# Performance work log

Measured on AMD Instinct MI355X. Metric: run time of the kernel, lower is better.

The kernel has to match this reference:

```python
import jax, jax.numpy as jnp
import numpy as np

B, S, D = 1, 4096, 512      # batch, seq, model dim
E, K, H = 64, 2, 256        # routed experts, top-k, expert hidden (moe_inter_dim)
HS = 2048                   # shared expert hidden = n_shared_experts * inter_dim
EPS = 1e-5                  # LayerNorm eps (torch default)


def setup_inputs() -> dict:
    key = jax.random.key(0)
    ks = jax.random.split(key, 16)
    n = lambda k, shp, s=0.02: jax.random.normal(k, shp, dtype=jnp.float32) * s
    return {
        "x": jax.random.normal(ks[0], (B, S, D), dtype=jnp.float32),
        # gate Linear(dim -> E)
        "Wg": n(ks[1], (E, D)), "bg": n(ks[2], (E,)),
        # per-expert LayerNorm affine
        "gamma": 1.0 + n(ks[3], (E, D)), "beta": n(ks[4], (E, D)),
        # per-expert SwiGLU: w1, w3: D->H ; w2: H->D
        "W1": n(ks[5], (E, D, H)), "b1": n(ks[6], (E, H)),
        "W3": n(ks[7], (E, D, H)), "b3": n(ks[8], (E, H)),
        "W2": n(ks[9], (E, H, D)), "b2": n(ks[10], (E, D)),
        # shared expert (same Expert structure, hidden HS)
        "gs": 1.0 + n(ks[11], (D,)), "bs": n(ks[11], (D,)),
        "Ws1": n(ks[12], (D, HS)), "bs1": n(ks[12], (HS,)),
        "Ws3": n(ks[13], (D, HS)), "bs3": n(ks[13], (HS,)),
        "Ws2": n(ks[14], (HS, D)), "bs2": n(ks[15], (D,)),
    }


def reference(x, Wg, bg, gamma, beta, W1, b1, W3, b3, W2, b2,
              gs, bs, Ws1, bs1, Ws3, bs3, Ws2, bs2):
    shape = x.shape
    xt = x.reshape(-1, D)                      # [T, D] tokens
    T = xt.shape[0]

    # ---- Gate (eval path: sigmoid scores, no load balancing / bias / groups) ----
    scores = jax.nn.sigmoid(xt @ Wg.T + bg)    # [T, E]
    w, idx = jax.lax.top_k(scores, K)          # [T, K]
    w = w / w.sum(-1, keepdims=True)           # sigmoid path normalization; route_scale = 1
    # dense combine weights: cw[t, e] = routing weight of token t on expert e (0 if not routed)
    cw = jnp.zeros((T, E), xt.dtype).at[jnp.arange(T)[:, None], idx].add(w)

    # ---- Shared LayerNorm statistics (affine folded per-expert below) ----
    mu = xt.mean(-1, keepdims=True)
    var = ((xt - mu) ** 2).mean(-1, keepdims=True)
    nx = (xt - mu) * jax.lax.rsqrt(var + EPS)  # [T, D], unit-affine normalized

    # Fold each expert's LN affine (gamma_e, beta_e) into its w1/w3:
    # (nx*g + b) @ W = nx @ (g[:,None]*W) + b @ W
    W1p = gamma[:, :, None] * W1
    b1p = b1 + jnp.einsum('ed,edh->eh', beta, W1)
    W3p = gamma[:, :, None] * W3
    b3p = b3 + jnp.einsum('ed,edh->eh', beta, W3)

    h1 = jnp.einsum('td,edh->eth', nx, W1p) + b1p[:, None, :]   # [E, T, H]
    h3 = jnp.einsum('td,edh->eth', nx, W3p) + b3p[:, None, :]
    h = jax.nn.silu(h1) * h3                                     # SwiGLU, [E, T, H]

    # Weighted combine: y[t] = sum_e cw[t,e] * (h[e,t] @ W2[e] + b2[e])
    hw = h * cw.T[:, :, None]                                    # [E, T, H]
    y = jnp.einsum('eth,ehd->td', hw, W2) + cw @ b2              # [T, D]

    # ---- Shared expert (applied to every token) ----
    nxs = nx * gs + bs
    hs = jax.nn.silu(nxs @ Ws1 + bs1) * (nxs @ Ws3 + bs3)        # [T, HS]
    z = hs @ Ws2 + bs2

    return (y + z).reshape(shape)
```

## Files before the change

### kernel.cpp

```cpp
#include <hip/hip_runtime.h>
#include <math.h>

typedef unsigned short u16;
typedef __attribute__((ext_vector_type(8))) short bf16x8;
typedef __attribute__((ext_vector_type(4))) float f32x4;

#define TT   4096
#define DM   512
#define NE   64
#define HE   256
#define HSH  2048
#define NSH  8
#define PADBASE 16384
#define MAXTILES 384
#define MAXRT    128

__device__ __forceinline__ float sig_(float z){ return 1.f/(1.f+__expf(-z)); }

__device__ __forceinline__ u16 f2bf(float x){
  unsigned int u = __builtin_bit_cast(unsigned int, x);
  u = (u + 0x7FFFu + ((u >> 16) & 1u)) >> 16;
  return (u16)u;
}

__device__ __forceinline__ f32x4 mfma16(bf16x8 a, bf16x8 b, f32x4 c){
  return __builtin_amdgcn_mfma_f32_16x16x32_bf16(a, b, c, 0, 0, 0);
}

__device__ __forceinline__ bf16x8 frd(const char* tile, int row, int q){
  return *(const bf16x8*)(tile + row*64 + q*16);
}

__device__ __forceinline__ void gl16(const void* g, void* l){
  __builtin_amdgcn_global_load_lds(
      (const __attribute__((address_space(1))) unsigned int*)g,
      (__attribute__((address_space(3))) unsigned int*)l, 16, 0, 0);
}

__global__ __launch_bounds__(256) void k_cvtT(
    const float* __restrict__ in, const float* __restrict__ scale,
    const float* __restrict__ foldvec, u16* __restrict__ out,
    float* __restrict__ foldout, int K, int N)
{
  __shared__ u16 T[64][80];
  __shared__ float red[64][65];
  const int tid = threadIdx.x;
  const int k0 = blockIdx.x*64, n0 = blockIdx.y*64;
  const float* ip = in + (size_t)blockIdx.z * K * N;
  const int r = tid>>2, cb = (tid&3)*16;
  const float sc = scale   ? scale[(size_t)blockIdx.z*K + k0 + r]   : 1.0f;
  const float fv = foldvec ? foldvec[(size_t)blockIdx.z*K + k0 + r] : 0.0f;
  #pragma unroll
  for (int j = 0; j < 4; j++){
    float4 v = *(const float4*)(ip + (size_t)(k0+r)*N + n0 + cb + j*4);
    T[cb+j*4+0][r] = f2bf(v.x*sc);
    T[cb+j*4+1][r] = f2bf(v.y*sc);
    T[cb+j*4+2][r] = f2bf(v.z*sc);
    T[cb+j*4+3][r] = f2bf(v.w*sc);
    if (foldout){
      red[cb+j*4+0][r] = v.x*fv;
      red[cb+j*4+1][r] = v.y*fv;
      red[cb+j*4+2][r] = v.z*fv;
      red[cb+j*4+3][r] = v.w*fv;
    }
  }
  __syncthreads();
  if (foldout){
    const int c = tid & 63, rq = tid >> 6;
    float s = 0.f;
    #pragma unroll
    for (int rr = 0; rr < 16; rr++) s += red[c][rq*16 + rr];
    atomicAdd(foldout + (size_t)blockIdx.z*N + n0 + c, s);
  }
  const int n = tid>>2, kb = (tid&3)*16;
  uint4 a = *(const uint4*)&T[n][kb];
  uint4 b = *(const uint4*)&T[n][kb+8];
  u16* op = out + (size_t)blockIdx.z*K*N;
  *(uint4*)(op + (size_t)(n0+n)*K + k0 + kb)     = a;
  *(uint4*)(op + (size_t)(n0+n)*K + k0 + kb + 8) = b;
}

__global__ __launch_bounds__(256) void k_ln_gate(
    const float* __restrict__ x, const float* __restrict__ Wg, const float* __restrict__ bg,
    u16* __restrict__ nxb, int* __restrict__ top_idx, float* __restrict__ top_w)
{
  __shared__ float xs[DM];
  __shared__ float sred[4], ssred[4];
  __shared__ float sc[NE];
  const int tid = threadIdx.x;
  const int t   = blockIdx.x;

  float2 v = reinterpret_cast<const float2*>(x + (size_t)t*DM)[tid];
  xs[2*tid]   = v.x;
  xs[2*tid+1] = v.y;
  float s  = v.x + v.y;
  float ss = v.x*v.x + v.y*v.y;
  #pragma unroll
  for (int o = 32; o > 0; o >>= 1){ s += __shfl_xor(s, o); ss += __shfl_xor(ss, o); }
  const int wid = tid >> 6, lane = tid & 63;
  if (lane == 0){ sred[wid] = s; ssred[wid] = ss; }
  __syncthreads();
  const float tot = sred[0]+sred[1]+sred[2]+sred[3];
  const float tss = ssred[0]+ssred[1]+ssred[2]+ssred[3];
  const float mu  = tot * (1.f/DM);
  const float var = tss * (1.f/DM) - mu*mu;
  const float rstd = rsqrtf(var + 1e-5f);
  unsigned int pk = (unsigned int)f2bf((v.x-mu)*rstd) | ((unsigned int)f2bf((v.y-mu)*rstd) << 16);
  *(unsigned int*)(nxb + (size_t)t*DM + 2*tid) = pk;

  const int e = tid >> 2, sub = tid & 3;
  const float4* wrow4 = reinterpret_cast<const float4*>(Wg + (size_t)e*DM);
  const float4* xs4   = reinterpret_cast<const float4*>(xs);
  float acc = 0.f;
  #pragma unroll 4
  for (int i = sub; i < DM/4; i += 4){
    const float4 w = wrow4[i]; const float4 xv = xs4[i];
    acc += xv.x*w.x + xv.y*w.y + xv.z*w.z + xv.w*w.w;
  }
  acc += __shfl_xor(acc, 1);
  acc += __shfl_xor(acc, 2);
  if (sub == 0) sc[e] = acc + bg[e];
  __syncthreads();

  if (tid < 64) {
    const float s0 = sc[tid];
    float m = s0; int mi = tid;
    #pragma unroll
    for (int o = 1; o < 64; o <<= 1){
      float om = __shfl_xor(m, o); int oi = __shfl_xor(mi, o);
      if (om > m || (om == m && oi < mi)) { m = om; mi = oi; }
    }
    float s1 = (tid == mi) ? -INFINITY : s0;
    float m2 = s1; int mi2 = tid;
    #pragma unroll
    for (int o = 1; o < 64; o <<= 1){
      float om = __shfl_xor(m2, o); int oi = __shfl_xor(mi2, o);
      if (om > m2 || (om == m2 && oi < mi2)) { m2 = om; mi2 = oi; }
    }
    if (tid == 0){
      const float w0 = sig_(m), w1 = sig_(m2);
      const float inv = 1.f/(w0+w1);
      top_idx[2*t]   = mi;
      top_idx[2*t+1] = mi2;
      top_w[2*t]     = w0*inv;
      top_w[2*t+1]   = w1*inv;
    }
  }
}

__global__ __launch_bounds__(256) void k_route(
    const int* __restrict__ top_idx, const float* __restrict__ top_w,
    int* __restrict__ bucket_tok, float* __restrict__ bucket_w,
    int* __restrict__ tiles, int* __restrict__ n_tiles)
{
  __shared__ int cnt[NE], base_[NE];
  __shared__ int nroute;
  const int tid = threadIdx.x;
  if (tid < NE) cnt[tid] = 0;
  __syncthreads();
  for (int p = tid; p < TT*2; p += 256) atomicAdd(&cnt[top_idx[p]], 1);
  __syncthreads();
  if (tid == 0){
    int run = 0, ntl = 0;
    for (int e = 0; e < NE; e++){
      base_[e] = run;
      const int c = cnt[e];
      for (int b = 0; b < c; b += 128){
        const int n = (c - b < 128) ? (c - b) : 128;
        tiles[ntl++] = (e << 17) | (((run + b) >> 7) << 8) | n;
      }
      run += ((c + 127) >> 7) << 7;
    }
    nroute = ntl;
    n_tiles[0] = ntl + NSH*(TT/128);
    n_tiles[1] = ntl;
  }
  __syncthreads();
  if (tid < NSH*(TT/128)){
    const int s = tid >> 5, t = tid & 31;
    const int b0 = PADBASE + s*TT + t*128;
    tiles[nroute + tid] = ((NE + s) << 17) | ((b0 >> 7) << 8) | 128;
  }
  if (tid < NE) cnt[tid] = 0;
  __syncthreads();
  for (int p = tid; p < TT*2; p += 256){
    const int e = top_idx[p];
    const int pos = base_[e] + atomicAdd(&cnt[e], 1);
    bucket_tok[pos] = p >> 1;
    bucket_w[pos]   = top_w[p];
  }
}

__global__ __launch_bounds__(512) void k_up(
    const u16* __restrict__ nxb,
    const u16* __restrict__ W1bT, const u16* __restrict__ W3bT,
    const u16* __restrict__ Ws1bT, const u16* __restrict__ Ws3bT,
    const float* __restrict__ b1, const float* __restrict__ b3,
    const float* __restrict__ bs1, const float* __restrict__ bs3,
    const float* __restrict__ b1f, const float* __restrict__ b3f,
    const int* __restrict__ bucket_tok, const float* __restrict__ bucket_w,
    const int* __restrict__ tiles, const int* __restrict__ n_tiles,
    u16* __restrict__ hrout, u16* __restrict__ hs)
{
  if ((int)blockIdx.x >= n_tiles[0]) return;
  const int info = tiles[blockIdx.x];
  const int e  = info >> 17;
  const int b0 = ((info >> 8) & 0x1FF) << 7;
  const int nt = info & 255;
  const bool sh = (e >= NE);
  const int y  = blockIdx.y;

  __shared__ __align__(16) char Ab[2][8192];
  __shared__ __align__(16) char B1b[2][8192];
  __shared__ __align__(16) char B3b[2][8192];
  __shared__ int   toks[128];
  __shared__ float tw[128];

  const int tid = threadIdx.x, wid = tid >> 6, lane = tid & 63;
  const int l15 = lane & 15, q = lane >> 4;

  if (tid < 128){
    int tk; float w;
    if (!sh){
      if (tid < nt){ tk = bucket_tok[b0+tid]; w = bucket_w[b0+tid]; }
      else         { tk = 0; w = 0.f; }
    } else {
      tk = ((b0 - PADBASE) & (TT-1)) + tid; w = 1.f;
    }
    toks[tid] = tk; tw[tid] = w;
  }
  __syncthreads();

  const u16* w1e = sh ? (Ws1bT + (size_t)(e-NE)*HE*DM) : (W1bT + (size_t)e*HE*DM);
  const u16* w3e = sh ? (Ws3bT + (size_t)(e-NE)*HE*DM) : (W3bT + (size_t)e*HE*DM);

  const int srow = lane >> 2, soff = (lane & 3)*8;
  const u16* asrc = nxb + (size_t)toks[wid*16 + srow]*DM + soff;
  const u16* b1s  = w1e + (size_t)(y*128 + wid*16 + srow)*DM + soff;
  const u16* b3s  = w3e + (size_t)(y*128 + wid*16 + srow)*DM + soff;
  const int loff = wid*1024;

#define UP_STAGE(ph, k0) do{ \
    gl16(asrc + (k0), Ab[ph] + loff); \
    gl16(b1s  + (k0), B1b[ph] + loff); \
    gl16(b3s  + (k0), B3b[ph] + loff); \
  } while(0)

  const int wm = (wid & 1)*64, wn = (wid >> 1)*32;

  const float* ob1 = sh ? (bs1 + (size_t)(e-NE)*HE) : (b1 + (size_t)e*HE);
  const float* ob3 = sh ? (bs3 + (size_t)(e-NE)*HE) : (b3 + (size_t)e*HE);
  f32x4 acc1[4][2], acc3[4][2];
  #pragma unroll
  for (int fn = 0; fn < 2; fn++){
    const int h = y*128 + wn + fn*16 + l15;
    const float v1 = ob1[h] + b1f[(size_t)e*HE + h];
    const float v3 = ob3[h] + b3f[(size_t)e*HE + h];
    #pragma unroll
    for (int fm = 0; fm < 4; fm++){
      acc1[fm][fn] = (f32x4){v1,v1,v1,v1};
      acc3[fm][fn] = (f32x4){v3,v3,v3,v3};
    }
  }

  UP_STAGE(0, 0);
  __syncthreads();

  for (int ks = 0; ks < DM/32; ks++){
    const int cur = ks & 1;
    if (ks < DM/32 - 1) UP_STAGE(cur^1, (ks+1)*32);
    const char* A  = Ab[cur];
    const char* B1 = B1b[cur];
    const char* B3 = B3b[cur];
    bf16x8 fa[4];
    #pragma unroll
    for (int fm = 0; fm < 4; fm++) fa[fm] = frd(A, wm + fm*16 + l15, q);
    #pragma unroll
    for (int fn = 0; fn < 2; fn++){
      bf16x8 fb1 = frd(B1, wn + fn*16 + l15, q);
      bf16x8 fb3 = frd(B3, wn + fn*16 + l15, q);
      #pragma unroll
      for (int fm = 0; fm < 4; fm++){
        acc1[fm][fn] = mfma16(fa[fm], fb1, acc1[fm][fn]);
        acc3[fm][fn] = mfma16(fa[fm], fb3, acc3[fm][fn]);
      }
    }
    __syncthreads();
  }
#undef UP_STAGE

  const int tbase = sh ? ((b0 - PADBASE) & (TT-1)) : 0;
  const int scol  = sh ? (e - NE)*HE : 0;
  #pragma unroll
  for (int fm = 0; fm < 4; fm++){
    #pragma unroll
    for (int fn = 0; fn < 2; fn++){
      const int hl = y*128 + wn + fn*16 + l15;
      #pragma unroll
      for (int r = 0; r < 4; r++){
        const int m = wm + fm*16 + 4*q + r;
        float v = 0.f;
        if (m < nt){
          const float a1 = acc1[fm][fn][r];
          const float a3 = acc3[fm][fn][r];
          v = a1 * sig_(a1) * a3 * tw[m];
        }
        if (sh) hs[(size_t)(tbase+m)*HSH + scol + hl] = f2bf(v);
        else    hrout[(size_t)(b0+m)*HE + hl] = f2bf(v);
      }
    }
  }
}

__global__ __launch_bounds__(256) void k_down_shared(
    const u16* __restrict__ hs, const u16* __restrict__ Ws2bT,
    const float* __restrict__ bs2, float* __restrict__ out)
{
  __shared__ __align__(16) char Ab[2][4096];
  __shared__ __align__(16) char Bb[2][8192];

  const int tid = threadIdx.x, wid = tid >> 6, lane = tid & 63;
  const int l15 = lane & 15, q = lane >> 4;
  const int t0 = blockIdx.x*64, d0 = blockIdx.y*128;

  const int srow = tid >> 2, soff = (tid & 3)*8;
  const u16* asrc  = hs    + (size_t)(t0 + srow)*HSH + soff;
  const u16* bsrc0 = Ws2bT + (size_t)(d0 + srow)*HSH + soff;
  const u16* bsrc1 = Ws2bT + (size_t)(d0 + 64 + srow)*HSH + soff;
  const int loff = wid*1024;

#define DS_STAGE(ph, k0) do{ \
    gl16(asrc  + (k0), Ab[ph] + loff); \
    gl16(bsrc0 + (k0), Bb[ph] + loff); \
    gl16(bsrc1 + (k0), Bb[ph] + 4096 + loff); \
  } while(0)

  const int wm = (wid & 1)*32, wn = (wid >> 1)*64;

  f32x4 acc[2][4];
  #pragma unroll
  for (int fm = 0; fm < 2; fm++)
    #pragma unroll
    for (int fn = 0; fn < 4; fn++) acc[fm][fn] = (f32x4){0.f,0.f,0.f,0.f};

  DS_STAGE(0, 0);
  __syncthreads();

  for (int ks = 0; ks < HSH/32; ks++){
    const int cur = ks & 1;
    if (ks < HSH/32 - 1) DS_STAGE(cur^1, (ks+1)*32);
    const char* A = Ab[cur];
    const char* B = Bb[cur];
    bf16x8 fa[2];
    #pragma unroll
    for (int fm = 0; fm < 2; fm++) fa[fm] = frd(A, wm + fm*16 + l15, q);
    #pragma unroll
    for (int fn = 0; fn < 4; fn++){
      bf16x8 fb = frd(B, wn + fn*16 + l15, q);
      #pragma unroll
      for (int fm = 0; fm < 2; fm++)
        acc[fm][fn] = mfma16(fa[fm], fb, acc[fm][fn]);
    }
    __syncthreads();
  }
#undef DS_STAGE

  #pragma unroll
  for (int fm = 0; fm < 2; fm++){
    #pragma unroll
    for (int fn = 0; fn < 4; fn++){
      const int d = d0 + wn + fn*16 + l15;
      const float bv = bs2[d];
      #pragma unroll
      for (int r = 0; r < 4; r++){
        const int t = t0 + wm + fm*16 + 4*q + r;
        out[(size_t)t*DM + d] = acc[fm][fn][r] + bv;
      }
    }
  }
}

__global__ __launch_bounds__(512) void k_down_routed(
    const u16* __restrict__ hrout, const u16* __restrict__ W2bT,
    const float* __restrict__ b2,
    const int* __restrict__ bucket_tok, const float* __restrict__ bucket_w,
    const int* __restrict__ tiles, const int* __restrict__ n_tiles,
    float* __restrict__ out)
{
  if ((int)blockIdx.x >= n_tiles[1]) return;
  const int info = tiles[blockIdx.x];
  const int e  = info >> 17;
  const int b0 = ((info >> 8) & 0x1FF) << 7;
  const int nt = info & 255;
  const int d0 = blockIdx.y * 256;

  __shared__ __align__(16) char Ab[2][8192];
  __shared__ __align__(16) char Bb[2][16384];
  __shared__ int   toks[128];
  __shared__ float tw[128];

  const int tid = threadIdx.x, wid = tid >> 6, lane = tid & 63;
  const int l15 = lane & 15, q = lane >> 4;

  if (tid < 128){
    if (tid < nt){ toks[tid] = bucket_tok[b0+tid]; tw[tid] = bucket_w[b0+tid]; }
    else         { toks[tid] = 0; tw[tid] = 0.f; }
  }
  __syncthreads();

  const u16* w2e = W2bT + (size_t)e*DM*HE;
  const int srow = tid >> 2, soff = (tid & 3)*8;
  const u16* asrc  = hrout + (size_t)(b0 + srow)*HE + soff;
  const u16* bsrc0 = w2e + (size_t)(d0 + srow)*HE + soff;
  const u16* bsrc1 = w2e + (size_t)(d0 + 128 + srow)*HE + soff;
  const int loff = wid*1024;

#define DR_STAGE(ph, k0) do{ \
    gl16(asrc  + (k0), Ab[ph] + loff); \
    gl16(bsrc0 + (k0), Bb[ph] + loff); \
    gl16(bsrc1 + (k0), Bb[ph] + 8192 + loff); \
  } while(0)

  const int wm = (wid & 1)*64, wn = (wid >> 1)*64;

  f32x4 acc[4][4];
  #pragma unroll
  for (int fm = 0; fm < 4; fm++)
    #pragma unroll
    for (int fn = 0; fn < 4; fn++) acc[fm][fn] = (f32x4){0.f,0.f,0.f,0.f};

  DR_STAGE(0, 0);
  __syncthreads();

  for (int ks = 0; ks < HE/32; ks++){
    const int cur = ks & 1;
    if (ks < HE/32 - 1) DR_STAGE(cur^1, (ks+1)*32);
    const char* A = Ab[cur];
    const char* B = Bb[cur];
    bf16x8 fa[4];
    #pragma unroll
    for (int fm = 0; fm < 4; fm++) fa[fm] = frd(A, wm + fm*16 + l15, q);
    #pragma unroll
    for (int fn = 0; fn < 4; fn++){
      bf16x8 fb = frd(B, wn + fn*16 + l15, q);
      #pragma unroll
      for (int fm = 0; fm < 4; fm++)
        acc[fm][fn] = mfma16(fa[fm], fb, acc[fm][fn]);
    }
    __syncthreads();
  }
#undef DR_STAGE

  #pragma unroll
  for (int fm = 0; fm < 4; fm++){
    #pragma unroll
    for (int fn = 0; fn < 4; fn++){
      const int d = d0 + wn + fn*16 + l15;
      #pragma unroll
      for (int r = 0; r < 4; r++){
        const int m = wm + fm*16 + 4*q + r;
        if (m < nt)
          atomicAdd(out + (size_t)toks[m]*DM + d, acc[fm][fn][r] + tw[m]*b2[(size_t)e*DM + d]);
      }
    }
  }
}

extern "C" void kernel_launch(void* const* d_in, const int* in_sizes, int n_in,
                              void* d_out, int out_size, void* d_ws, size_t ws_size,
                              hipStream_t stream)
{
  (void)in_sizes; (void)n_in; (void)ws_size; (void)out_size;
  const float* x     = (const float*)d_in[0];
  const float* Wg    = (const float*)d_in[1];
  const float* bg    = (const float*)d_in[2];
  const float* gamma = (const float*)d_in[3];
  const float* beta  = (const float*)d_in[4];
  const float* W1    = (const float*)d_in[5];
  const float* b1    = (const float*)d_in[6];
  const float* W3    = (const float*)d_in[7];
  const float* b3    = (const float*)d_in[8];
  const float* W2    = (const float*)d_in[9];
  const float* b2    = (const float*)d_in[10];
  const float* gs    = (const float*)d_in[11];
  const float* bs    = (const float*)d_in[12];
  const float* Ws1   = (const float*)d_in[13];
  const float* bs1   = (const float*)d_in[14];
  const float* Ws3   = (const float*)d_in[15];
  const float* bs3   = (const float*)d_in[16];
  const float* Ws2   = (const float*)d_in[17];
  const float* bs2   = (const float*)d_in[18];
  float* out = (float*)d_out;

  char* ws = (char*)d_ws;
  size_t off = 0;
  auto alloc = [&](size_t bytes) -> char* {
    char* p = ws + off;
    off += (bytes + 255) & ~(size_t)255;
    return p;
  };
  u16*   nxb        = (u16*)  alloc((size_t)TT*DM*2);
  int*   top_idx    = (int*)  alloc((size_t)TT*2*4);
  float* top_w      = (float*)alloc((size_t)TT*2*4);
  int*   bucket_tok = (int*)  alloc((size_t)PADBASE*4);
  float* bucket_w   = (float*)alloc((size_t)PADBASE*4);
  int*   tiles      = (int*)  alloc(MAXTILES*4);
  int*   n_tiles    = (int*)  alloc(64);
  u16*   hrout      = (u16*)  alloc((size_t)PADBASE*HE*2);
  u16*   hs         = (u16*)  alloc((size_t)TT*HSH*2);
  u16*   W1bT       = (u16*)  alloc((size_t)NE*HE*DM*2);
  u16*   W3bT       = (u16*)  alloc((size_t)NE*HE*DM*2);
  u16*   W2bT       = (u16*)  alloc((size_t)NE*DM*HE*2);
  u16*   Ws1bT      = (u16*)  alloc((size_t)HSH*DM*2);
  u16*   Ws3bT      = (u16*)  alloc((size_t)HSH*DM*2);
  u16*   Ws2bT      = (u16*)  alloc((size_t)DM*HSH*2);
  float* b1f        = (float*)alloc((size_t)(NE*HE + HSH)*4);
  float* b3f        = (float*)alloc((size_t)(NE*HE + HSH)*4);

  hipMemsetAsync(b1f, 0, (size_t)(NE*HE + HSH)*4, stream);
  hipMemsetAsync(b3f, 0, (size_t)(NE*HE + HSH)*4, stream);
  k_cvtT<<<dim3(DM/64, HE/64, NE), 256, 0, stream>>>(W1, gamma, beta, W1bT, b1f, DM, HE);
  k_cvtT<<<dim3(DM/64, HE/64, NE), 256, 0, stream>>>(W3, gamma, beta, W3bT, b3f, DM, HE);
  k_cvtT<<<dim3(HE/64, DM/64, NE), 256, 0, stream>>>(W2, nullptr, nullptr, W2bT, nullptr, HE, DM);
  k_cvtT<<<dim3(DM/64, HSH/64, 1), 256, 0, stream>>>(Ws1, gs, bs, Ws1bT, b1f + NE*HE, DM, HSH);
  k_cvtT<<<dim3(DM/64, HSH/64, 1), 256, 0, stream>>>(Ws3, gs, bs, Ws3bT, b3f + NE*HE, DM, HSH);
  k_cvtT<<<dim3(HSH/64, DM/64, 1), 256, 0, stream>>>(Ws2, nullptr, nullptr, Ws2bT, nullptr, HSH, DM);

  k_ln_gate<<<dim3(TT), 256, 0, stream>>>(x, Wg, bg, nxb, top_idx, top_w);
  k_route<<<dim3(1), 256, 0, stream>>>(top_idx, top_w, bucket_tok, bucket_w, tiles, n_tiles);

  k_up<<<dim3(MAXTILES, 2), 512, 0, stream>>>(nxb, W1bT, W3bT, Ws1bT, Ws3bT,
                                              b1, b3, bs1, bs3, b1f, b3f,
                                              bucket_tok, bucket_w, tiles, n_tiles, hrout, hs);
  k_down_shared<<<dim3(TT/64, DM/128), 256, 0, stream>>>(hs, Ws2bT, bs2, out);
  k_down_routed<<<dim3(MAXRT, 2), 512, 0, stream>>>(hrout, W2bT, b2,
                                                    bucket_tok, bucket_w, tiles, n_tiles, out);
}
```

Before: 226.1 us.

## Triple-buffer GEMM loads, swizzle LDS tiles, fuse weight conversion launches

Each of the three GEMM kernels now keeps three LDS stages in flight. It waits with explicit vmcnt counts and raw barriers instead of __syncthreads, and raises wave priority around the MFMA block, so global loads overlap compute more deeply. The LDS column index is XOR-swizzled on both the global-to-LDS copy and the fragment reads to reduce bank conflicts. The six weight conversion/transposition launches are merged into one grid that dispatches by block index, cutting launch overhead. These changes raise LDS use per block, which may lower occupancy, and they depend on hand-counted waitcnt values being correct.

Result: faster. 204.9 us (-9.4%).

```diff
diff --git a/kernel.cpp b/kernel.cpp
--- a/kernel.cpp
+++ b/kernel.cpp
@@ -15,6 +15,10 @@
 #define MAXTILES 384
 #define MAXRT    128
 
+#define WAITV(N) asm volatile("s_waitcnt vmcnt(" #N ")" ::: "memory")
+#define SBAR()   __builtin_amdgcn_s_barrier()
+#define SCHEDB() __builtin_amdgcn_sched_barrier(0)
+
 __device__ __forceinline__ float sig_(float z){ return 1.f/(1.f+__expf(-z)); }
 
 __device__ __forceinline__ u16 f2bf(float x){
@@ -27,8 +31,8 @@
   return __builtin_amdgcn_mfma_f32_16x16x32_bf16(a, b, c, 0, 0, 0);
 }
 
-__device__ __forceinline__ bf16x8 frd(const char* tile, int row, int q){
-  return *(const bf16x8*)(tile + row*64 + q*16);
+__device__ __forceinline__ bf16x8 frd(const char* tile, int row, int csw){
+  return *(const bf16x8*)(tile + row*64 + csw);
 }
 
 __device__ __forceinline__ void gl16(const void* g, void* l){
@@ -37,47 +41,61 @@
       (__attribute__((address_space(3))) unsigned int*)l, 16, 0, 0);
 }
 
-__global__ __launch_bounds__(256) void k_cvtT(
-    const float* __restrict__ in, const float* __restrict__ scale,
-    const float* __restrict__ foldvec, u16* __restrict__ out,
-    float* __restrict__ foldout, int K, int N)
-{
+struct CvtJob {
+  const float* in; const float* scale; const float* fvec;
+  u16* out; float* fout; int K; int N; int base;
+};
+struct CvtJobs { CvtJob j[6]; };
+
+__global__ __launch_bounds__(256) void k_cvt_all(CvtJobs jobs)
+{
+  const int bid = blockIdx.x;
+  int ji = 0;
+  #pragma unroll
+  for (int i = 1; i < 6; i++) ji = (bid >= jobs.j[i].base) ? i : ji;
+  const CvtJob J = jobs.j[ji];
+  const int local = bid - J.base;
+  const int nbx = J.K >> 6, nby = J.N >> 6;
+  const int pm = nbx * nby;
+  const int z = local / pm, rem = local - z*pm;
+  const int bx = rem % nbx, by = rem / nbx;
+
   __shared__ u16 T[64][80];
   __shared__ float red[64][65];
   const int tid = threadIdx.x;
-  const int k0 = blockIdx.x*64, n0 = blockIdx.y*64;
-  const float* ip = in + (size_t)blockIdx.z * K * N;
+  const int k0 = bx*64, n0 = by*64;
+  const float* ip = J.in + (size_t)z * J.K * J.N;
   const int r = tid>>2, cb = (tid&3)*16;
-  const float sc = scale   ? scale[(size_t)blockIdx.z*K + k0 + r]   : 1.0f;
-  const float fv = foldvec ? foldvec[(size_t)blockIdx.z*K + k0 + r] : 0.0f;
-  #pragma unroll
-  for (int j = 0; j < 4; j++){
-    float4 v = *(const float4*)(ip + (size_t)(k0+r)*N + n0 + cb + j*4);
-    T[cb+j*4+0][r] = f2bf(v.x*sc);
-    T[cb+j*4+1][r] = f2bf(v.y*sc);
-    T[cb+j*4+2][r] = f2bf(v.z*sc);
-    T[cb+j*4+3][r] = f2bf(v.w*sc);
-    if (foldout){
-      red[cb+j*4+0][r] = v.x*fv;
-      red[cb+j*4+1][r] = v.y*fv;
-      red[cb+j*4+2][r] = v.z*fv;
-      red[cb+j*4+3][r] = v.w*fv;
-    }
-  }
-  __syncthreads();
-  if (foldout){
+  const float sc = J.scale ? J.scale[(size_t)z*J.K + k0 + r] : 1.0f;
+  const float fv = J.fvec  ? J.fvec [(size_t)z*J.K + k0 + r] : 0.0f;
+  #pragma unroll
+  for (int jj = 0; jj < 4; jj++){
+    float4 v = *(const float4*)(ip + (size_t)(k0+r)*J.N + n0 + cb + jj*4);
+    T[cb+jj*4+0][r] = f2bf(v.x*sc);
+    T[cb+jj*4+1][r] = f2bf(v.y*sc);
+    T[cb+jj*4+2][r] = f2bf(v.z*sc);
+    T[cb+jj*4+3][r] = f2bf(v.w*sc);
+    if (J.fout){
+      red[cb+jj*4+0][r] = v.x*fv;
+      red[cb+jj*4+1][r] = v.y*fv;
+      red[cb+jj*4+2][r] = v.z*fv;
+      red[cb+jj*4+3][r] = v.w*fv;
+    }
+  }
+  __syncthreads();
+  if (J.fout){
     const int c = tid & 63, rq = tid >> 6;
     float s = 0.f;
     #pragma unroll
     for (int rr = 0; rr < 16; rr++) s += red[c][rq*16 + rr];
-    atomicAdd(foldout + (size_t)blockIdx.z*N + n0 + c, s);
+    atomicAdd(J.fout + (size_t)z*J.N + n0 + c, s);
   }
   const int n = tid>>2, kb = (tid&3)*16;
   uint4 a = *(const uint4*)&T[n][kb];
   uint4 b = *(const uint4*)&T[n][kb+8];
-  u16* op = out + (size_t)blockIdx.z*K*N;
-  *(uint4*)(op + (size_t)(n0+n)*K + k0 + kb)     = a;
-  *(uint4*)(op + (size_t)(n0+n)*K + k0 + kb + 8) = b;
+  u16* op = J.out + (size_t)z*J.K*J.N;
+  *(uint4*)(op + (size_t)(n0+n)*J.K + k0 + kb)     = a;
+  *(uint4*)(op + (size_t)(n0+n)*J.K + k0 + kb + 8) = b;
 }
 
 __global__ __launch_bounds__(256) void k_ln_gate(
@@ -210,9 +228,9 @@
   const bool sh = (e >= NE);
   const int y  = blockIdx.y;
 
-  __shared__ __align__(16) char Ab[2][8192];
-  __shared__ __align__(16) char B1b[2][8192];
-  __shared__ __align__(16) char B3b[2][8192];
+  __shared__ __align__(16) char Ab[3][8192];
+  __shared__ __align__(16) char B1b[3][8192];
+  __shared__ __align__(16) char B3b[3][8192];
   __shared__ int   toks[128];
   __shared__ float tw[128];
 
@@ -234,10 +252,11 @@
   const u16* w1e = sh ? (Ws1bT + (size_t)(e-NE)*HE*DM) : (W1bT + (size_t)e*HE*DM);
   const u16* w3e = sh ? (Ws3bT + (size_t)(e-NE)*HE*DM) : (W3bT + (size_t)e*HE*DM);
 
-  const int srow = lane >> 2, soff = (lane & 3)*8;
-  const u16* asrc = nxb + (size_t)toks[wid*16 + srow]*DM + soff;
-  const u16* b1s  = w1e + (size_t)(y*128 + wid*16 + srow)*DM + soff;
-  const u16* b3s  = w3e + (size_t)(y*128 + wid*16 + srow)*DM + soff;
+  const int srow = lane >> 2;
+  const int csrc = (((lane & 3) ^ ((lane >> 3) & 3))) * 8;
+  const u16* asrc = nxb + (size_t)toks[wid*16 + srow]*DM + csrc;
+  const u16* b1s  = w1e + (size_t)(y*128 + wid*16 + srow)*DM + csrc;
+  const u16* b3s  = w3e + (size_t)(y*128 + wid*16 + srow)*DM + csrc;
   const int loff = wid*1024;
 
 #define UP_STAGE(ph, k0) do{ \
@@ -264,28 +283,36 @@
   }
 
   UP_STAGE(0, 0);
-  __syncthreads();
+  UP_STAGE(1, 32);
+  const int csw = (q ^ ((l15 >> 1) & 3)) * 16;
 
   for (int ks = 0; ks < DM/32; ks++){
-    const int cur = ks & 1;
-    if (ks < DM/32 - 1) UP_STAGE(cur^1, (ks+1)*32);
+    const int cur = ks % 3;
+    if (ks + 2 < DM/32) UP_STAGE((ks+2)%3, (ks+2)*32);
+    if (ks < DM/32 - 2)       WAITV(6);
+    else if (ks == DM/32 - 2) WAITV(3);
+    else                      WAITV(0);
+    SBAR();
+    __builtin_amdgcn_s_setprio(1);
     const char* A  = Ab[cur];
     const char* B1 = B1b[cur];
     const char* B3 = B3b[cur];
     bf16x8 fa[4];
     #pragma unroll
-    for (int fm = 0; fm < 4; fm++) fa[fm] = frd(A, wm + fm*16 + l15, q);
+    for (int fm = 0; fm < 4; fm++) fa[fm] = frd(A, wm + fm*16 + l15, csw);
     #pragma unroll
     for (int fn = 0; fn < 2; fn++){
-      bf16x8 fb1 = frd(B1, wn + fn*16 + l15, q);
-      bf16x8 fb3 = frd(B3, wn + fn*16 + l15, q);
+      bf16x8 fb1 = frd(B1, wn + fn*16 + l15, csw);
+      bf16x8 fb3 = frd(B3, wn + fn*16 + l15, csw);
       #pragma unroll
       for (int fm = 0; fm < 4; fm++){
         acc1[fm][fn] = mfma16(fa[fm], fb1, acc1[fm][fn]);
         acc3[fm][fn] = mfma16(fa[fm], fb3, acc3[fm][fn]);
       }
     }
-    __syncthreads();
+    __builtin_amdgcn_s_setprio(0);
+    SCHEDB();
+    SBAR();
   }
 #undef UP_STAGE
 
@@ -316,17 +343,18 @@
     const u16* __restrict__ hs, const u16* __restrict__ Ws2bT,
     const float* __restrict__ bs2, float* __restrict__ out)
 {
-  __shared__ __align__(16) char Ab[2][4096];
-  __shared__ __align__(16) char Bb[2][8192];
+  __shared__ __align__(16) char Ab[3][4096];
+  __shared__ __align__(16) char Bb[3][8192];
 
   const int tid = threadIdx.x, wid = tid >> 6, lane = tid & 63;
   const int l15 = lane & 15, q = lane >> 4;
   const int t0 = blockIdx.x*64, d0 = blockIdx.y*128;
 
-  const int srow = tid >> 2, soff = (tid & 3)*8;
-  const u16* asrc  = hs    + (size_t)(t0 + srow)*HSH + soff;
-  const u16* bsrc0 = Ws2bT + (size_t)(d0 + srow)*HSH + soff;
-  const u16* bsrc1 = Ws2bT + (size_t)(d0 + 64 + srow)*HSH + soff;
+  const int srow = tid >> 2;
+  const int csrc = (((tid & 3) ^ ((tid >> 3) & 3))) * 8;
+  const u16* asrc  = hs    + (size_t)(t0 + srow)*HSH + csrc;
+  const u16* bsrc0 = Ws2bT + (size_t)(d0 + srow)*HSH + csrc;
+  const u16* bsrc1 = Ws2bT + (size_t)(d0 + 64 + srow)*HSH + csrc;
   const int loff = wid*1024;
 
 #define DS_STAGE(ph, k0) do{ \
@@ -344,24 +372,32 @@
     for (int fn = 0; fn < 4; fn++) acc[fm][fn] = (f32x4){0.f,0.f,0.f,0.f};
 
   DS_STAGE(0, 0);
-  __syncthreads();
+  DS_STAGE(1, 32);
+  const int csw = (q ^ ((l15 >> 1) & 3)) * 16;
 
   for (int ks = 0; ks < HSH/32; ks++){
-    const int cur = ks & 1;
-    if (ks < HSH/32 - 1) DS_STAGE(cur^1, (ks+1)*32);
+    const int cur = ks % 3;
+    if (ks + 2 < HSH/32) DS_STAGE((ks+2)%3, (ks+2)*32);
+    if (ks < HSH/32 - 2)       WAITV(6);
+    else if (ks == HSH/32 - 2) WAITV(3);
+    else                       WAITV(0);
+    SBAR();
+    __builtin_amdgcn_s_setprio(1);
     const char* A = Ab[cur];
     const char* B = Bb[cur];
     bf16x8 fa[2];
     #pragma unroll
-    for (int fm = 0; fm < 2; fm++) fa[fm] = frd(A, wm + fm*16 + l15, q);
+    for (int fm = 0; fm < 2; fm++) fa[fm] = frd(A, wm + fm*16 + l15, csw);
     #pragma unroll
     for (int fn = 0; fn < 4; fn++){
-      bf16x8 fb = frd(B, wn + fn*16 + l15, q);
+      bf16x8 fb = frd(B, wn + fn*16 + l15, csw);
       #pragma unroll
       for (int fm = 0; fm < 2; fm++)
         acc[fm][fn] = mfma16(fa[fm], fb, acc[fm][fn]);
     }
-    __syncthreads();
+    __builtin_amdgcn_s_setprio(0);
+    SCHEDB();
+    SBAR();
   }
 #undef DS_STAGE
 
@@ -394,8 +430,8 @@
   const int nt = info & 255;
   const int d0 = blockIdx.y * 256;
 
-  __shared__ __align__(16) char Ab[2][8192];
-  __shared__ __align__(16) char Bb[2][16384];
+  __shared__ __align__(16) char Ab[3][8192];
+  __shared__ __align__(16) char Bb[3][16384];
   __shared__ int   toks[128];
   __shared__ float tw[128];
 
@@ -409,10 +445,11 @@
   __syncthreads();
 
   const u16* w2e = W2bT + (size_t)e*DM*HE;
-  const int srow = tid >> 2, soff = (tid & 3)*8;
-  const u16* asrc  = hrout + (size_t)(b0 + srow)*HE + soff;
-  const u16* bsrc0 = w2e + (size_t)(d0 + srow)*HE + soff;
-  const u16* bsrc1 = w2e + (size_t)(d0 + 128 + srow)*HE + soff;
+  const int srow = tid >> 2;
+  const int csrc = (((tid & 3) ^ ((tid >> 3) & 3))) * 8;
+  const u16* asrc  = hrout + (size_t)(b0 + srow)*HE + csrc;
+  const u16* bsrc0 = w2e + (size_t)(d0 + srow)*HE + csrc;
+  const u16* bsrc1 = w2e + (size_t)(d0 + 128 + srow)*HE + csrc;
   const int loff = wid*1024;
 
 #define DR_STAGE(ph, k0) do{ \
@@ -430,24 +467,32 @@
     for (int fn = 0; fn < 4; fn++) acc[fm][fn] = (f32x4){0.f,0.f,0.f,0.f};
 
   DR_STAGE(0, 0);
-  __syncthreads();
+  DR_STAGE(1, 32);
+  const int csw = (q ^ ((l15 >> 1) & 3)) * 16;
 
   for (int ks = 0; ks < HE/32; ks++){
-    const int cur = ks & 1;
-    if (ks < HE/32 - 1) DR_STAGE(cur^1, (ks+1)*32);
+    const int cur = ks % 3;
+    if (ks + 2 < HE/32) DR_STAGE((ks+2)%3, (ks+2)*32);
+    if (ks < HE/32 - 2)       WAITV(6);
+    else if (ks == HE/32 - 2) WAITV(3);
+    else                      WAITV(0);
+    SBAR();
+    __builtin_amdgcn_s_setprio(1);
     const char* A = Ab[cur];
     const char* B = Bb[cur];
     bf16x8 fa[4];
     #pragma unroll
-    for (int fm = 0; fm < 4; fm++) fa[fm] = frd(A, wm + fm*16 + l15, q);
+    for (int fm = 0; fm < 4; fm++) fa[fm] = frd(A, wm + fm*16 + l15, csw);
     #pragma unroll
     for (int fn = 0; fn < 4; fn++){
-      bf16x8 fb = frd(B, wn + fn*16 + l15, q);
+      bf16x8 fb = frd(B, wn + fn*16 + l15, csw);
       #pragma unroll
       for (int fm = 0; fm < 4; fm++)
         acc[fm][fn] = mfma16(fa[fm], fb, acc[fm][fn]);
     }
-    __syncthreads();
+    __builtin_amdgcn_s_setprio(0);
+    SCHEDB();
+    SBAR();
   }
 #undef DR_STAGE
 
@@ -519,12 +564,14 @@
 
   hipMemsetAsync(b1f, 0, (size_t)(NE*HE + HSH)*4, stream);
   hipMemsetAsync(b3f, 0, (size_t)(NE*HE + HSH)*4, stream);
-  k_cvtT<<<dim3(DM/64, HE/64, NE), 256, 0, stream>>>(W1, gamma, beta, W1bT, b1f, DM, HE);
-  k_cvtT<<<dim3(DM/64, HE/64, NE), 256, 0, stream>>>(W3, gamma, beta, W3bT, b3f, DM, HE);
-  k_cvtT<<<dim3(HE/64, DM/64, NE), 256, 0, stream>>>(W2, nullptr, nullptr, W2bT, nullptr, HE, DM);
-  k_cvtT<<<dim3(DM/64, HSH/64, 1), 256, 0, stream>>>(Ws1, gs, bs, Ws1bT, b1f + NE*HE, DM, HSH);
-  k_cvtT<<<dim3(DM/64, HSH/64, 1), 256, 0, stream>>>(Ws3, gs, bs, Ws3bT, b3f + NE*HE, DM, HSH);
-  k_cvtT<<<dim3(HSH/64, DM/64, 1), 256, 0, stream>>>(Ws2, nullptr, nullptr, Ws2bT, nullptr, HSH, DM);
+  CvtJobs jobs;
+  jobs.j[0] = { W1,  gamma, beta, W1bT,  b1f,          DM,  HE,  0    };
+  jobs.j[1] = { W3,  gamma, beta, W3bT,  b3f,          DM,  HE,  2048 };
+  jobs.j[2] = { W2,  nullptr, nullptr, W2bT, nullptr,  HE,  DM,  4096 };
+  jobs.j[3] = { Ws1, gs, bs, Ws1bT, b1f + NE*HE,       DM,  HSH, 6144 };
+  jobs.j[4] = { Ws3, gs, bs, Ws3bT, b3f + NE*HE,       DM,  HSH, 6400 };
+  jobs.j[5] = { Ws2, nullptr, nullptr, Ws2bT, nullptr, HSH, DM,  6656 };
+  k_cvt_all<<<dim3(6912), 256, 0, stream>>>(jobs);
 
   k_ln_gate<<<dim3(TT), 256, 0, stream>>>(x, Wg, bg, nxb, top_idx, top_w);
   k_route<<<dim3(1), 256, 0, stream>>>(top_idx, top_w, bucket_tok, bucket_w, tiles, n_tiles);
```
